# Kernel optimization log

Hardware: AMD Instinct MI355X
Metric: run time of the kernel (lower is better)

## Reference

```python
import jax, jax.numpy as jnp
import numpy as np

EPS = 1e-08

def setup_inputs() -> dict:
    key = jax.random.key(0)
    x = jax.random.normal(key, (16, 2048), dtype=jnp.float32)  # [B, L]
    return {"x": x}

def reference(x) -> jnp.ndarray:
    # min-max normalize per series to [-1, 1]
    min_x = jnp.min(x, axis=1, keepdims=True)
    max_x = jnp.max(x, axis=1, keepdims=True)
    scaled = 2.0 * ((x - min_x) / (max_x - min_x + EPS)) - 1.0
    scaled = jnp.clip(scaled, -1.0 + EPS, 1.0 - EPS)
    phi = jnp.arccos(scaled)                      # [B, L]
    gaf = jnp.cos(phi[:, :, None] + phi[:, None, :])  # [B, L, L]
    return gaf
```

## Files before the change

### kernel.cpp

```cpp
#include <hip/hip_runtime.h>
#include <hip/hip_bf16.h>
#include <math.h>

#define L 2048
#define NB 16
#define ROWS_PER_BLOCK 16
#define THREADS 256
#define GAF_EPS 1e-8f

__global__ __launch_bounds__(THREADS) void gaf_kernel(const float* __restrict__ x,
                                                      float* __restrict__ out) {
    __shared__ float sc[L];
    __shared__ float ss[L];
    __shared__ float red[8];

    const int chunks_per_batch = L / ROWS_PER_BLOCK;
    const int b = blockIdx.x / chunks_per_batch;
    const int i0 = (blockIdx.x % chunks_per_batch) * ROWS_PER_BLOCK;
    const int t = threadIdx.x;
    const float* __restrict__ xrow = x + (size_t)b * L;

    float v[8];
    float mn = INFINITY, mx = -INFINITY;
#pragma unroll
    for (int k = 0; k < 8; ++k) {
        v[k] = xrow[t + k * THREADS];
        mn = fminf(mn, v[k]);
        mx = fmaxf(mx, v[k]);
    }
#pragma unroll
    for (int off = 32; off > 0; off >>= 1) {
        mn = fminf(mn, __shfl_down(mn, off));
        mx = fmaxf(mx, __shfl_down(mx, off));
    }
    const int wave = t >> 6;
    if ((t & 63) == 0) { red[wave] = mn; red[4 + wave] = mx; }
    __syncthreads();
    if (t == 0) {
        red[0] = fminf(fminf(red[0], red[1]), fminf(red[2], red[3]));
        red[4] = fmaxf(fmaxf(red[4], red[5]), fmaxf(red[6], red[7]));
    }
    __syncthreads();
    mn = red[0];
    mx = red[4];
    const float inv = 1.0f / (mx - mn + GAF_EPS);

#pragma unroll
    for (int k = 0; k < 8; ++k) {
        float c = 2.0f * ((v[k] - mn) * inv) - 1.0f;
        c = fminf(fmaxf(c, -1.0f + GAF_EPS), 1.0f - GAF_EPS);
        const int idx = t + k * THREADS;
        sc[idx] = c;
        ss[idx] = sqrtf(fmaxf(1.0f - c * c, 0.0f));
    }
    __syncthreads();

    float* __restrict__ obase = out + ((size_t)b * L + (size_t)i0) * L;
#pragma unroll
    for (int i = 0; i < ROWS_PER_BLOCK; ++i) {
        const float ci = sc[i0 + i];
        const float si = ss[i0 + i];
        float4* __restrict__ orow = (float4*)(obase + (size_t)i * L);
#pragma unroll
        for (int it = 0; it < L / (4 * THREADS); ++it) {
            const int j4 = t + it * THREADS;
            const float4 cj = ((const float4*)sc)[j4];
            const float4 sj = ((const float4*)ss)[j4];
            float4 o;
            o.x = ci * cj.x - si * sj.x;
            o.y = ci * cj.y - si * sj.y;
            o.z = ci * cj.z - si * sj.z;
            o.w = ci * cj.w - si * sj.w;
            orow[j4] = o;
        }
    }
}

extern "C" void kernel_launch(void* const* d_in, const int* in_sizes, int n_in,
                              void* d_out, int out_size, void* d_ws, size_t ws_size,
                              hipStream_t stream) {
    const float* x = (const float*)d_in[0];
    float* out = (float*)d_out;
    const dim3 grid(NB * (L / ROWS_PER_BLOCK));
    gaf_kernel<<<grid, THREADS, 0, stream>>>(x, out);
}
```

Before: 253.9 us.

## Split prep into separate kernel and stream output with nontemporal stores

Moves the per-series min/max and the cos/sin computation into a small prep kernel that writes to workspace. The main kernel then only loads its column vectors and row scalars into registers and writes the output with nontemporal stores. Before, every one of the 2048 blocks repeated the reduction and the shared-memory setup. The cost is a second kernel launch and a dependency through global memory.

```diff
diff --git a/kernel.cpp b/kernel.cpp
--- a/kernel.cpp
+++ b/kernel.cpp
@@ -8,15 +8,13 @@
 #define THREADS 256
 #define GAF_EPS 1e-8f
 
-__global__ __launch_bounds__(THREADS) void gaf_kernel(const float* __restrict__ x,
-                                                      float* __restrict__ out) {
-    __shared__ float sc[L];
-    __shared__ float ss[L];
+typedef float f32x4 __attribute__((ext_vector_type(4)));
+
+
+__global__ __launch_bounds__(THREADS) void gaf_prep(const float* __restrict__ x,
+                                                    float* __restrict__ ws) {
     __shared__ float red[8];
-
-    const int chunks_per_batch = L / ROWS_PER_BLOCK;
-    const int b = blockIdx.x / chunks_per_batch;
-    const int i0 = (blockIdx.x % chunks_per_batch) * ROWS_PER_BLOCK;
+    const int b = blockIdx.x;
     const int t = threadIdx.x;
     const float* __restrict__ xrow = x + (size_t)b * L;
 
@@ -45,34 +43,48 @@
     mx = red[4];
     const float inv = 1.0f / (mx - mn + GAF_EPS);
 
+    float* __restrict__ cb = ws + (size_t)b * 2 * L;
+    float* __restrict__ sb = cb + L;
 #pragma unroll
     for (int k = 0; k < 8; ++k) {
         float c = 2.0f * ((v[k] - mn) * inv) - 1.0f;
         c = fminf(fmaxf(c, -1.0f + GAF_EPS), 1.0f - GAF_EPS);
         const int idx = t + k * THREADS;
-        sc[idx] = c;
-        ss[idx] = sqrtf(fmaxf(1.0f - c * c, 0.0f));
+        cb[idx] = c;
+        sb[idx] = sqrtf(fmaxf(1.0f - c * c, 0.0f));
     }
-    __syncthreads();
+}
 
-    float* __restrict__ obase = out + ((size_t)b * L + (size_t)i0) * L;
+__global__ __launch_bounds__(THREADS) void gaf_stream(const float* __restrict__ ws,
+                                                      float* __restrict__ out) {
+    const int b = blockIdx.x >> 7;
+    const int i0 = (blockIdx.x & 127) << 4;
+    const int t = threadIdx.x;
+
+    const float* __restrict__ cb = ws + (size_t)b * 2 * L;
+    const float* __restrict__ sb = cb + L;
+
+    const f32x4 cj0 = ((const f32x4*)cb)[t];
+    const f32x4 cj1 = ((const f32x4*)cb)[t + THREADS];
+    const f32x4 sj0 = ((const f32x4*)sb)[t];
+    const f32x4 sj1 = ((const f32x4*)sb)[t + THREADS];
+
+    float ci[ROWS_PER_BLOCK], si[ROWS_PER_BLOCK];
 #pragma unroll
     for (int i = 0; i < ROWS_PER_BLOCK; ++i) {
-        const float ci = sc[i0 + i];
-        const float si = ss[i0 + i];
-        float4* __restrict__ orow = (float4*)(obase + (size_t)i * L);
+        ci[i] = cb[i0 + i];
+        si[i] = sb[i0 + i];
+    }
+
+    float* __restrict__ ob = out + ((size_t)b * L + (size_t)i0) * L;
 #pragma unroll
-        for (int it = 0; it < L / (4 * THREADS); ++it) {
-            const int j4 = t + it * THREADS;
-            const float4 cj = ((const float4*)sc)[j4];
-            const float4 sj = ((const float4*)ss)[j4];
-            float4 o;
-            o.x = ci * cj.x - si * sj.x;
-            o.y = ci * cj.y - si * sj.y;
-            o.z = ci * cj.z - si * sj.z;
-            o.w = ci * cj.w - si * sj.w;
-            orow[j4] = o;
-        }
+    for (int i = 0; i < ROWS_PER_BLOCK; ++i) {
+        const float c = ci[i], s = si[i];
+        const f32x4 o0 = c * cj0 - s * sj0;
+        const f32x4 o1 = c * cj1 - s * sj1;
+        f32x4* __restrict__ orow = (f32x4*)(ob + (size_t)i * L);
+        __builtin_nontemporal_store(o0, orow + t);
+        __builtin_nontemporal_store(o1, orow + t + THREADS);
     }
 }
 
@@ -81,6 +93,7 @@
                               hipStream_t stream) {
     const float* x = (const float*)d_in[0];
     float* out = (float*)d_out;
-    const dim3 grid(NB * (L / ROWS_PER_BLOCK));
-    gaf_kernel<<<grid, THREADS, 0, stream>>>(x, out);
+    float* ws = (float*)d_ws;
+    gaf_prep<<<dim3(NB), THREADS, 0, stream>>>(x, ws);
+    gaf_stream<<<dim3(NB * (L / ROWS_PER_BLOCK)), THREADS, 0, stream>>>(ws, out);
 }
```

Result: slower. 266.6 us (+5.0%).
